# Kernel optimization log

Hardware: AMD Instinct MI355X
Metric: run time of the kernel (lower is better)

Reference implementation:

```python
import jax, jax.numpy as jnp
import numpy as np

MAX_REL_IDX = 32
N_REL_POS = 2 * MAX_REL_IDX + 1  # 65
ATTN_DIM = 8


def setup_inputs() -> dict:
    key = jax.random.key(0)
    kW, kb = jax.random.split(key)
    B, N = 4, 2048
    index = jnp.arange(B * N, dtype=jnp.int32).reshape(B, N)
    W = jax.random.normal(kW, (ATTN_DIM, N_REL_POS), dtype=jnp.float32) * 0.1
    b = jax.random.normal(kb, (ATTN_DIM,), dtype=jnp.float32) * 0.1
    return {"index": index, "W": W, "b": b}


def reference(index, W, b):
    # d_ij[b,i,j] = index[b,i] - index[b,j]
    d_ij = index[..., :, None] - index[..., None, :]            # [B,N,N] int
    # argmin_k |d_ij - (k - max_rel)| == clip(d_ij, -max, max) + max
    idxs = jnp.clip(d_ij + MAX_REL_IDX, 0, N_REL_POS - 1)        # [B,N,N]
    # one_hot(idxs) @ W^T + b  ==  gather rows of W^T
    table = W.T                                                  # [n_rel_pos, attn_dim]
    return table[idxs] + b                                       # [B,N,N,attn_dim]
```

## Files before the change

kernel.cpp:

```cpp
#include <hip/hip_runtime.h>


#define MAX_REL 32
#define NRP 65
#define AD 8

typedef float f4 __attribute__((ext_vector_type(4)));

__global__ __launch_bounds__(256) void relpos_kernel(
    const int* __restrict__ index,
    const float* __restrict__ W,
    const float* __restrict__ bias,
    float* __restrict__ out,
    int N)
{
    extern __shared__ char smem[];
    float* s_tabf = (float*)smem;
    f4*    s_tab4 = (f4*)smem;
    int*   s_idx  = (int*)(smem + NRP * AD * sizeof(float));

    const int tid = threadIdx.x;
    const int i   = blockIdx.x;
    const int bb  = blockIdx.y;

    for (int t = tid; t < NRP * AD; t += 256) {
        int p = t >> 3;
        int k = t & 7;
        s_tabf[t] = W[k * NRP + p] + bias[k];
    }
    const int* irow = index + (size_t)bb * (size_t)N;
    for (int t = tid; t < N; t += 256) {
        s_idx[t] = irow[t];
    }
    __syncthreads();

    const int idx_i = s_idx[i];
    const int vecs  = N * 2;
    f4* orow = (f4*)(out + ((size_t)bb * (size_t)N + (size_t)i) * (size_t)N * AD);

    for (int f = tid; f < vecs; f += 256) {
        int j = f >> 1;
        int c = idx_i - s_idx[j] + MAX_REL;
        c = c < 0 ? 0 : (c > NRP - 1 ? NRP - 1 : c);
        f4 v = s_tab4[c * 2 + (f & 1)];
        __builtin_nontemporal_store(v, &orow[f]);
    }
}

extern "C" void kernel_launch(void* const* d_in, const int* in_sizes, int n_in,
                              void* d_out, int out_size, void* d_ws, size_t ws_size,
                              hipStream_t stream) {
    const int*   index = (const int*)d_in[0];
    const float* W     = (const float*)d_in[1];
    const float* bias  = (const float*)d_in[2];
    float*       out   = (float*)d_out;

    const long long BN = in_sizes[0];
    const long long N  = (long long)out_size / (BN * AD);
    const long long B  = BN / N;

    const size_t smem = NRP * AD * sizeof(float) + (size_t)N * sizeof(int);
    dim3 grid((unsigned)N, (unsigned)B, 1);
    relpos_kernel<<<grid, 256, smem, stream>>>(index, W, bias, out, (int)N);
}
```

Baseline: 113.3 us.

## Process multiple output rows per block and cache column indices in registers

Each block now writes eight output rows instead of one. The lookup table and index row are loaded into shared memory once per block, which amortises that setup and the barrier over more work. When the row width matches exactly, the per-thread column indices are preloaded into a register array and reused for every row. The trade-offs are fewer blocks, which means less parallelism, and more registers per thread.

```diff
diff --git a/kernel.cpp b/kernel.cpp
--- a/kernel.cpp
+++ b/kernel.cpp
@@ -4,10 +4,13 @@
 #define MAX_REL 32
 #define NRP 65
 #define AD 8
+#define ROWS 8
+#define BLK 256
+#define SLOTS 16
 
 typedef float f4 __attribute__((ext_vector_type(4)));
 
-__global__ __launch_bounds__(256) void relpos_kernel(
+__global__ __launch_bounds__(BLK) void relpos_kernel(
     const int* __restrict__ index,
     const float* __restrict__ W,
     const float* __restrict__ bias,
@@ -20,30 +23,57 @@
     int*   s_idx  = (int*)(smem + NRP * AD * sizeof(float));
 
     const int tid = threadIdx.x;
-    const int i   = blockIdx.x;
+    const int i0  = blockIdx.x * ROWS;
     const int bb  = blockIdx.y;
 
-    for (int t = tid; t < NRP * AD; t += 256) {
+    for (int t = tid; t < NRP * AD; t += BLK) {
         int p = t >> 3;
         int k = t & 7;
         s_tabf[t] = W[k * NRP + p] + bias[k];
     }
     const int* irow = index + (size_t)bb * (size_t)N;
-    for (int t = tid; t < N; t += 256) {
+    for (int t = tid; t < N; t += BLK) {
         s_idx[t] = irow[t];
     }
     __syncthreads();
 
-    const int idx_i = s_idx[i];
-    const int vecs  = N * 2;
-    f4* orow = (f4*)(out + ((size_t)bb * (size_t)N + (size_t)i) * (size_t)N * AD);
+    const int vecs = N * 2;
+    f4* obase = (f4*)out + ((size_t)bb * (size_t)N + (size_t)i0) * (size_t)(N * 2);
 
-    for (int f = tid; f < vecs; f += 256) {
-        int j = f >> 1;
-        int c = idx_i - s_idx[j] + MAX_REL;
-        c = c < 0 ? 0 : (c > NRP - 1 ? NRP - 1 : c);
-        f4 v = s_tab4[c * 2 + (f & 1)];
-        __builtin_nontemporal_store(v, &orow[f]);
+    if (vecs == SLOTS * BLK) {
+        int sj[SLOTS];
+        #pragma unroll
+        for (int k = 0; k < SLOTS; ++k)
+            sj[k] = s_idx[(tid + k * BLK) >> 1];
+
+        #pragma unroll
+        for (int r = 0; r < ROWS; ++r) {
+            const int i = i0 + r;
+            if (i >= N) break;
+            const int idx_i = s_idx[i] + MAX_REL;
+            f4* orow = obase + (size_t)r * (size_t)vecs;
+            #pragma unroll
+            for (int k = 0; k < SLOTS; ++k) {
+                const int f = tid + k * BLK;
+                int c = idx_i - sj[k];
+                c = c < 0 ? 0 : (c > NRP - 1 ? NRP - 1 : c);
+                f4 v = s_tab4[c * 2 + (f & 1)];
+                __builtin_nontemporal_store(v, &orow[f]);
+            }
+        }
+    } else {
+        for (int r = 0; r < ROWS; ++r) {
+            const int i = i0 + r;
+            if (i >= N) break;
+            const int idx_i = s_idx[i] + MAX_REL;
+            f4* orow = obase + (size_t)r * (size_t)vecs;
+            for (int f = tid; f < vecs; f += BLK) {
+                int c = idx_i - s_idx[f >> 1];
+                c = c < 0 ? 0 : (c > NRP - 1 ? NRP - 1 : c);
+                f4 v = s_tab4[c * 2 + (f & 1)];
+                __builtin_nontemporal_store(v, &orow[f]);
+            }
+        }
     }
 }
 
@@ -60,6 +90,6 @@
     const long long B  = BN / N;
 
     const size_t smem = NRP * AD * sizeof(float) + (size_t)N * sizeof(int);
-    dim3 grid((unsigned)N, (unsigned)B, 1);
-    relpos_kernel<<<grid, 256, smem, stream>>>(index, W, bias, out, (int)N);
+    dim3 grid((unsigned)((N + ROWS - 1) / ROWS), (unsigned)B, 1);
+    relpos_kernel<<<grid, BLK, smem, stream>>>(index, W, bias, out, (int)N);
 }
```

New measurement: 106.9 us. -5.6%, faster.
